# Kernel tuning notes

Measured on AMD Instinct MI355X. Metric: run time of the kernel, lower is better.

The kernel has to match this reference:

```python
import jax, jax.numpy as jnp
import numpy as np

B, T, DM, DK = 8, 2048, 1024, 64

def setup_inputs() -> dict:
    key = jax.random.key(0)
    kx, kk, kq, kv = jax.random.split(key, 4)
    s = 1.0 / np.sqrt(DM)
    return {
        "x": jax.random.normal(kx, (B, T, DM), dtype=jnp.float32),
        "Wk": jax.random.normal(kk, (DM, DK), dtype=jnp.float32) * s,
        "Wq": jax.random.normal(kq, (DM, DK), dtype=jnp.float32) * s,
        "Wv": jax.random.normal(kv, (DM, DK), dtype=jnp.float32) * s,
    }

def reference(x, Wk, Wq, Wv):
    # q, k, v: [B, T, DK]
    k = x @ Wk
    q = x @ Wq
    v = x @ Wv
    # NOTE: original module does NOT scale by 1/sqrt(dk)
    wei = jnp.einsum('btd,bsd->bts', q, k)          # [B, T, T]
    mask = jnp.tril(jnp.ones((x.shape[1], x.shape[1]), dtype=bool))
    wei = jnp.where(mask, wei, -jnp.inf)
    wei = jax.nn.softmax(wei, axis=-1)
    return wei @ v                                   # [B, T, DK]
```

## Files before the change

### kernel.cpp

```cpp
#include <hip/hip_runtime.h>
#include <hip/hip_bf16.h>

typedef unsigned short u16;
typedef __bf16 bf16x8 __attribute__((ext_vector_type(8)));
typedef _Float16 f16x8 __attribute__((ext_vector_type(8)));
typedef float f32x4 __attribute__((ext_vector_type(4)));

#define DEVINL __device__ __forceinline__

static constexpr int Bc = 8, Tc = 2048;

DEVINL u16 f2bf(float f) {
  unsigned u = __builtin_bit_cast(unsigned, f);
  unsigned r = u + 0x7fffu + ((u >> 16) & 1u);
  return (u16)(r >> 16);
}
DEVINL float bf2f(u16 h) {
  unsigned u = ((unsigned)h) << 16;
  return __builtin_bit_cast(float, u);
}

DEVINL bf16x8 lds_ld8(const u16* p, int row, int col) {
  return *(const bf16x8*)&p[row * 64 + (col ^ ((row & 7) << 3))];
}
DEVINL f16x8 lds_ld8h(const u16* p, int row, int col) {
  return *(const f16x8*)&p[row * 64 + (col ^ ((row & 7) << 3))];
}

__global__ __launch_bounds__(256) void build_wt(const float* __restrict__ Wk,
                                                const float* __restrict__ Wq,
                                                const float* __restrict__ Wv,
                                                u16* __restrict__ wt_s) {
  int idx = blockIdx.x * 256 + threadIdx.x;
  int ch = idx / 12288;
  int rem = idx - ch * 12288;
  int c = rem >> 6, kc = rem & 63;
  int k = ch * 64 + (kc ^ ((c & 7) << 3));
  const float* W = (c < 64) ? Wk : (c < 128 ? Wq : Wv);
  _Float16 h = (_Float16)W[k * 64 + (c & 63)];
  wt_s[idx] = __builtin_bit_cast(u16, h);
}

__global__ __launch_bounds__(256, 2) void proj_kernel(const float* __restrict__ x,
                                                      const u16* __restrict__ wt_s,
                                                      u16* __restrict__ kb,
                                                      u16* __restrict__ qb,
                                                      u16* __restrict__ vt) {
  __shared__ u16 wl[2][192 * 64];
  __shared__ u16 xl[2][32 * 64];
  const int t = threadIdx.x;
  const int w = t >> 6, lane = t & 63;
  const int l16 = lane & 15, lhi = lane >> 4;
  const int rb = blockIdx.x * 32;
  const int cb = w * 48;
  const int sr = t >> 3, sc = (t & 7) * 8;
  const f32x4* xrow = (const f32x4*)(x + (size_t)(rb + sr) * 1024 + sc);

  f32x4 acc[2][3];
#pragma unroll
  for (int a = 0; a < 2; ++a)
#pragma unroll
    for (int c = 0; c < 3; ++c) acc[a][c] = (f32x4){0.f, 0.f, 0.f, 0.f};

#define STAGE_WT(S, CH)                                                        \
  {                                                                            \
    const u16* src = wt_s + (size_t)(CH) * 12288 + t * 8;                      \
    u16* dst = &wl[S][t * 8];                                                  \
    _Pragma("unroll") for (int i = 0; i < 6; ++i)                              \
      __builtin_amdgcn_global_load_lds(                                        \
          (const __attribute__((address_space(1))) unsigned int*)(src + i * 2048), \
          (__attribute__((address_space(3))) unsigned int*)(dst + i * 2048),   \
          16, 0, 0);                                                           \
  }

#define CVT_STORE(S, F0, F1)                                                   \
  {                                                                            \
    union { _Float16 h[8]; uint4 v; } p_;                                      \
    _Pragma("unroll") for (int j = 0; j < 4; ++j) {                            \
      p_.h[j] = (_Float16)(F0)[j];                                             \
      p_.h[4 + j] = (_Float16)(F1)[j];                                         \
    }                                                                          \
    *(uint4*)&xl[S][sr * 64 + (sc ^ ((sr & 7) << 3))] = p_.v;                  \
  }

#define COMPUTE(S)                                                             \
  _Pragma("unroll") for (int kk = 0; kk < 2; ++kk) {                           \
    f16x8 a0 = lds_ld8h(xl[S], l16, kk * 32 + lhi * 8);                        \
    f16x8 a1 = lds_ld8h(xl[S], 16 + l16, kk * 32 + lhi * 8);                   \
    _Pragma("unroll") for (int tc = 0; tc < 3; ++tc) {                         \
      int c_ = cb + tc * 16 + l16;                                             \
      f16x8 bf = *(const f16x8*)&wl[S][c_ * 64 + ((kk * 32 + lhi * 8) ^ ((c_ & 7) << 3))]; \
      acc[0][tc] = __builtin_amdgcn_mfma_f32_16x16x32_f16(a0, bf, acc[0][tc], 0, 0, 0); \
      acc[1][tc] = __builtin_amdgcn_mfma_f32_16x16x32_f16(a1, bf, acc[1][tc], 0, 0, 0); \
    }                                                                          \
  }

  STAGE_WT(0, 0);
  {
    f32x4 A0 = __builtin_nontemporal_load(xrow);
    f32x4 A1 = __builtin_nontemporal_load(xrow + 1);
    CVT_STORE(0, A0, A1);
  }
  __syncthreads();

#pragma unroll 2
  for (int ch = 0; ch < 16; ++ch) {
    const int cur = ch & 1, nxt = cur ^ 1;
    f32x4 A0, A1;
    if (ch + 1 < 16) {
      STAGE_WT(nxt, ch + 1);
      A0 = __builtin_nontemporal_load(xrow + (ch + 1) * 16);
      A1 = __builtin_nontemporal_load(xrow + (ch + 1) * 16 + 1);
    }
    COMPUTE(cur);
    if (ch + 1 < 16) {
      CVT_STORE(nxt, A0, A1);
      __syncthreads();
    }
  }
#undef STAGE_WT
#undef CVT_STORE
#undef COMPUTE

#pragma unroll
  for (int ri = 0; ri < 2; ++ri) {
#pragma unroll
    for (int tc = 0; tc < 3; ++tc) {
      int gc = cb + tc * 16 + l16;
      int cc = gc & 63;
      int row = rb + ri * 16 + lhi * 4;
#pragma unroll
      for (int i = 0; i < 4; ++i) {
        float f = acc[ri][tc][i];
        int r = row + i;
        if (gc < 64) {
          _Float16 h = (_Float16)f;
          kb[(size_t)r * 64 + cc] = __builtin_bit_cast(u16, h);
        } else if (gc < 128) {
          _Float16 h = (_Float16)f;
          qb[(size_t)r * 64 + cc] = __builtin_bit_cast(u16, h);
        } else {
          int bb = r >> 11, tp = r & 2047;
          vt[((size_t)bb * 64 + cc) * 2048 + tp] = f2bf(f);
        }
      }
    }
  }
}

__global__ __launch_bounds__(256, 2) void attn_kernel(const u16* __restrict__ qb,
                                                      const u16* __restrict__ kb,
                                                      const u16* __restrict__ vt,
                                                      float* __restrict__ out) {
  __shared__ u16 p_l[4][2][1024];
  __shared__ float om[4][32][64];
  __shared__ float ml[4][2][32];

  const int t = threadIdx.x, w = t >> 6, lane = t & 63;
  const int l16 = lane & 15, lhi = lane >> 4;
  const int b = blockIdx.x & 7, j = 63 - (blockIdx.x >> 3);
  const int ntt = (j + 2) >> 1;
  const size_t qrow = (size_t)b * 2048 + j * 32;

  f16x8 aq[2][2];
#pragma unroll
  for (int rs = 0; rs < 2; ++rs)
#pragma unroll
    for (int kk = 0; kk < 2; ++kk) {
      size_t qo = (qrow + rs * 16 + l16) * 64 + kk * 32 + lhi * 8;
      aq[rs][kk] = *(const f16x8*)(qb + qo);
    }

  f32x4 o[2][4];
  float m_r[2][4], l_r[2][4];
#pragma unroll
  for (int rs = 0; rs < 2; ++rs)
#pragma unroll
    for (int i = 0; i < 4; ++i) {
      o[rs][i] = (f32x4){0.f, 0.f, 0.f, 0.f};
      m_r[rs][i] = -3.0e38f; l_r[rs][i] = 0.f;
    }

  for (int tk = w; tk < ntt; tk += 4) {
    const int kvb = tk * 64;
    const size_t kbase = ((size_t)b * 2048 + kvb) * 64;

    f32x4 sa[2][4];
#pragma unroll
    for (int t4 = 0; t4 < 4; ++t4) {
      size_t kr = kbase + (size_t)(t4 * 16 + l16) * 64 + lhi * 8;
      f16x8 kf0 = *(const f16x8*)(kb + kr);
      f16x8 kf1 = *(const f16x8*)(kb + kr + 32);
#pragma unroll
      for (int rs = 0; rs < 2; ++rs) {
        f32x4 s = (f32x4){0.f, 0.f, 0.f, 0.f};
        s = __builtin_amdgcn_mfma_f32_16x16x32_f16(aq[rs][0], kf0, s, 0, 0, 0);
        s = __builtin_amdgcn_mfma_f32_16x16x32_f16(aq[rs][1], kf1, s, 0, 0, 0);
        sa[rs][t4] = s;
      }
    }

    bf16x8 vv[4][2];
#pragma unroll
    for (int t4 = 0; t4 < 4; ++t4) {
      size_t vr = ((size_t)b * 64 + t4 * 16 + l16) * 2048 + kvb + lhi * 8;
      vv[t4][0] = *(const bf16x8*)(vt + vr);
      vv[t4][1] = *(const bf16x8*)(vt + vr + 32);
    }

    if (tk == ntt - 1) {
#pragma unroll
      for (int rs = 0; rs < 2; ++rs) {
        int qr = j * 32 + rs * 16 + lhi * 4;
#pragma unroll
        for (int t4 = 0; t4 < 4; ++t4) {
          int col = kvb + t4 * 16 + l16;
#pragma unroll
          for (int i = 0; i < 4; ++i)
            if (col > qr + i) sa[rs][t4][i] = -1e30f;
        }
      }
    }

#pragma unroll
    for (int rs = 0; rs < 2; ++rs) {
      float pf[4][4];
#pragma unroll
      for (int i = 0; i < 4; ++i) {
        float tm = fmaxf(fmaxf(sa[rs][0][i], sa[rs][1][i]), fmaxf(sa[rs][2][i], sa[rs][3][i]));
#pragma unroll
        for (int d = 1; d < 16; d <<= 1) tm = fmaxf(tm, __shfl_xor(tm, d));
        float mn = fmaxf(m_r[rs][i], tm);
        float scl = __expf(m_r[rs][i] - mn);
        float rsum = 0.f;
#pragma unroll
        for (int t4 = 0; t4 < 4; ++t4) {
          float p = __expf(sa[rs][t4][i] - mn);
          pf[t4][i] = p;
          rsum += p;
        }
#pragma unroll
        for (int d = 1; d < 16; d <<= 1) rsum += __shfl_xor(rsum, d);
        l_r[rs][i] = l_r[rs][i] * scl + rsum;
        m_r[rs][i] = mn;
#pragma unroll
        for (int t4 = 0; t4 < 4; ++t4) o[rs][t4][i] *= scl;
      }

      u16* pw = (u16*)p_l[w][rs];
#pragma unroll
      for (int i = 0; i < 4; ++i) {
        int rr = lhi * 4 + i;
#pragma unroll
        for (int t4 = 0; t4 < 4; ++t4) {
          int col = t4 * 16 + l16;
          pw[rr * 64 + (col ^ ((rr & 7) << 3))] = f2bf(pf[t4][i]);
        }
      }
#pragma unroll
      for (int kk = 0; kk < 2; ++kk) {
        bf16x8 ap = lds_ld8(pw, l16, kk * 32 + lhi * 8);
#pragma unroll
        for (int t4 = 0; t4 < 4; ++t4)
          o[rs][t4] = __builtin_amdgcn_mfma_f32_16x16x32_bf16(ap, vv[t4][kk], o[rs][t4], 0, 0, 0);
      }
    }
  }

#pragma unroll
  for (int rs = 0; rs < 2; ++rs)
#pragma unroll
    for (int t4 = 0; t4 < 4; ++t4) {
      int col = t4 * 16 + l16;
#pragma unroll
      for (int i = 0; i < 4; ++i)
        om[w][rs * 16 + lhi * 4 + i][col] = o[rs][t4][i];
    }
  if (l16 == 0) {
#pragma unroll
    for (int rs = 0; rs < 2; ++rs)
#pragma unroll
      for (int i = 0; i < 4; ++i) {
        int r = rs * 16 + lhi * 4 + i;
        ml[w][0][r] = m_r[rs][i];
        ml[w][1][r] = l_r[rs][i];
      }
  }
  __syncthreads();

  {
    int r = t >> 3, c0 = (t & 7) * 8;
    float m0 = ml[0][0][r], m1 = ml[1][0][r], m2 = ml[2][0][r], m3 = ml[3][0][r];
    float M = fmaxf(fmaxf(m0, m1), fmaxf(m2, m3));
    float a0 = __expf(m0 - M), a1 = __expf(m1 - M);
    float a2 = __expf(m2 - M), a3 = __expf(m3 - M);
    float den = ml[0][1][r] * a0 + ml[1][1][r] * a1 + ml[2][1][r] * a2 + ml[3][1][r] * a3;
    float inv = 1.f / den;
    float* og = out + (qrow + r) * 64 + c0;
#pragma unroll
    for (int cc = 0; cc < 8; ++cc) {
      float v = om[0][r][c0 + cc] * a0 + om[1][r][c0 + cc] * a1 +
                om[2][r][c0 + cc] * a2 + om[3][r][c0 + cc] * a3;
      og[cc] = v * inv;
    }
  }
}

extern "C" void kernel_launch(void* const* d_in, const int* in_sizes, int n_in,
                              void* d_out, int out_size, void* d_ws, size_t ws_size,
                              hipStream_t stream) {
  const float* x  = (const float*)d_in[0];
  const float* Wk = (const float*)d_in[1];
  const float* Wq = (const float*)d_in[2];
  const float* Wv = (const float*)d_in[3];
  float* out = (float*)d_out;

  const size_t QKV = (size_t)Bc * Tc * 64;
  char* w = (char*)d_ws;
  u16* kb   = (u16*)w;               w += QKV * 2;
  u16* qb   = (u16*)w;               w += QKV * 2;
  u16* vt   = (u16*)w;               w += QKV * 2;
  u16* wt_s = (u16*)w;               w += (size_t)16 * 192 * 64 * 2;

  build_wt<<<768, 256, 0, stream>>>(Wk, Wq, Wv, wt_s);
  proj_kernel<<<512, 256, 0, stream>>>(x, wt_s, kb, qb, vt);
  attn_kernel<<<512, 256, 0, stream>>>(qb, kb, vt, out);
}
```

Measured before the change: 67.34 us.

## Compute transposed scores so P stays in registers for the PV MFMA

Swaps the MFMA operand order so each lane holds scores for a single query row across four key positions. The probabilities can then feed a 16x16x16 f16 MFMA directly as register fragments, which removes the per-tile LDS round trip for P. V is now stored as f16 instead of bf16 to match. The row max and sum now need only two cross-lane shuffles instead of four, and the output staging buffer is padded to reduce bank conflicts. The cost is twice as many smaller MFMAs and narrower 4-element V loads.

```diff
diff --git a/kernel.cpp b/kernel.cpp
--- a/kernel.cpp
+++ b/kernel.cpp
@@ -4,6 +4,7 @@
 typedef unsigned short u16;
 typedef __bf16 bf16x8 __attribute__((ext_vector_type(8)));
 typedef _Float16 f16x8 __attribute__((ext_vector_type(8)));
+typedef _Float16 f16x4 __attribute__((ext_vector_type(4)));
 typedef float f32x4 __attribute__((ext_vector_type(4)));
 
 #define DEVINL __device__ __forceinline__
@@ -15,14 +16,7 @@
   unsigned r = u + 0x7fffu + ((u >> 16) & 1u);
   return (u16)(r >> 16);
 }
-DEVINL float bf2f(u16 h) {
-  unsigned u = ((unsigned)h) << 16;
-  return __builtin_bit_cast(float, u);
-}
-
-DEVINL bf16x8 lds_ld8(const u16* p, int row, int col) {
-  return *(const bf16x8*)&p[row * 64 + (col ^ ((row & 7) << 3))];
-}
+
 DEVINL f16x8 lds_ld8h(const u16* p, int row, int col) {
   return *(const f16x8*)&p[row * 64 + (col ^ ((row & 7) << 3))];
 }
@@ -133,15 +127,15 @@
       for (int i = 0; i < 4; ++i) {
         float f = acc[ri][tc][i];
         int r = row + i;
+        _Float16 h = (_Float16)f;
+        u16 hb = __builtin_bit_cast(u16, h);
         if (gc < 64) {
-          _Float16 h = (_Float16)f;
-          kb[(size_t)r * 64 + cc] = __builtin_bit_cast(u16, h);
+          kb[(size_t)r * 64 + cc] = hb;
         } else if (gc < 128) {
-          _Float16 h = (_Float16)f;
-          qb[(size_t)r * 64 + cc] = __builtin_bit_cast(u16, h);
+          qb[(size_t)r * 64 + cc] = hb;
         } else {
           int bb = r >> 11, tp = r & 2047;
-          vt[((size_t)bb * 64 + cc) * 2048 + tp] = f2bf(f);
+          vt[((size_t)bb * 64 + cc) * 2048 + tp] = hb;
         }
       }
     }
@@ -152,8 +146,7 @@
                                                       const u16* __restrict__ kb,
                                                       const u16* __restrict__ vt,
                                                       float* __restrict__ out) {
-  __shared__ u16 p_l[4][2][1024];
-  __shared__ float om[4][32][64];
+  __shared__ float om[4][32][65];
   __shared__ float ml[4][2][32];
 
   const int t = threadIdx.x, w = t >> 6, lane = t & 63;
@@ -172,14 +165,13 @@
     }
 
   f32x4 o[2][4];
-  float m_r[2][4], l_r[2][4];
-#pragma unroll
-  for (int rs = 0; rs < 2; ++rs)
-#pragma unroll
-    for (int i = 0; i < 4; ++i) {
-      o[rs][i] = (f32x4){0.f, 0.f, 0.f, 0.f};
-      m_r[rs][i] = -3.0e38f; l_r[rs][i] = 0.f;
-    }
+  float m_r[2], l_r[2];
+#pragma unroll
+  for (int rs = 0; rs < 2; ++rs) {
+    m_r[rs] = -3.0e38f; l_r[rs] = 0.f;
+#pragma unroll
+    for (int d4 = 0; d4 < 4; ++d4) o[rs][d4] = (f32x4){0.f, 0.f, 0.f, 0.f};
+  }
 
   for (int tk = w; tk < ntt; tk += 4) {
     const int kvb = tk * 64;
@@ -194,97 +186,87 @@
 #pragma unroll
       for (int rs = 0; rs < 2; ++rs) {
         f32x4 s = (f32x4){0.f, 0.f, 0.f, 0.f};
-        s = __builtin_amdgcn_mfma_f32_16x16x32_f16(aq[rs][0], kf0, s, 0, 0, 0);
-        s = __builtin_amdgcn_mfma_f32_16x16x32_f16(aq[rs][1], kf1, s, 0, 0, 0);
+        s = __builtin_amdgcn_mfma_f32_16x16x32_f16(kf0, aq[rs][0], s, 0, 0, 0);
+        s = __builtin_amdgcn_mfma_f32_16x16x32_f16(kf1, aq[rs][1], s, 0, 0, 0);
         sa[rs][t4] = s;
       }
     }
 
-    bf16x8 vv[4][2];
-#pragma unroll
-    for (int t4 = 0; t4 < 4; ++t4) {
-      size_t vr = ((size_t)b * 64 + t4 * 16 + l16) * 2048 + kvb + lhi * 8;
-      vv[t4][0] = *(const bf16x8*)(vt + vr);
-      vv[t4][1] = *(const bf16x8*)(vt + vr + 32);
+    f16x4 va[4][4];
+#pragma unroll
+    for (int d4 = 0; d4 < 4; ++d4) {
+      size_t vr = ((size_t)b * 64 + d4 * 16 + l16) * 2048 + kvb + lhi * 4;
+#pragma unroll
+      for (int t4 = 0; t4 < 4; ++t4)
+        va[d4][t4] = *(const f16x4*)(vt + vr + t4 * 16);
     }
 
     if (tk == ntt - 1) {
 #pragma unroll
       for (int rs = 0; rs < 2; ++rs) {
-        int qr = j * 32 + rs * 16 + lhi * 4;
+        int q = j * 32 + rs * 16 + l16;
 #pragma unroll
         for (int t4 = 0; t4 < 4; ++t4) {
-          int col = kvb + t4 * 16 + l16;
+          int kvr = kvb + t4 * 16 + lhi * 4;
 #pragma unroll
           for (int i = 0; i < 4; ++i)
-            if (col > qr + i) sa[rs][t4][i] = -1e30f;
+            if (kvr + i > q) sa[rs][t4][i] = -1e30f;
         }
       }
     }
 
+    f16x4 pfrag[2][4];
 #pragma unroll
     for (int rs = 0; rs < 2; ++rs) {
-      float pf[4][4];
-#pragma unroll
-      for (int i = 0; i < 4; ++i) {
-        float tm = fmaxf(fmaxf(sa[rs][0][i], sa[rs][1][i]), fmaxf(sa[rs][2][i], sa[rs][3][i]));
-#pragma unroll
-        for (int d = 1; d < 16; d <<= 1) tm = fmaxf(tm, __shfl_xor(tm, d));
-        float mn = fmaxf(m_r[rs][i], tm);
-        float scl = __expf(m_r[rs][i] - mn);
-        float rsum = 0.f;
-#pragma unroll
-        for (int t4 = 0; t4 < 4; ++t4) {
-          float p = __expf(sa[rs][t4][i] - mn);
-          pf[t4][i] = p;
-          rsum += p;
-        }
-#pragma unroll
-        for (int d = 1; d < 16; d <<= 1) rsum += __shfl_xor(rsum, d);
-        l_r[rs][i] = l_r[rs][i] * scl + rsum;
-        m_r[rs][i] = mn;
-#pragma unroll
-        for (int t4 = 0; t4 < 4; ++t4) o[rs][t4][i] *= scl;
+      float tm = fmaxf(fmaxf(fmaxf(sa[rs][0][0], sa[rs][0][1]), fmaxf(sa[rs][0][2], sa[rs][0][3])),
+                       fmaxf(fmaxf(sa[rs][1][0], sa[rs][1][1]), fmaxf(sa[rs][1][2], sa[rs][1][3])));
+      float tm2 = fmaxf(fmaxf(fmaxf(sa[rs][2][0], sa[rs][2][1]), fmaxf(sa[rs][2][2], sa[rs][2][3])),
+                        fmaxf(fmaxf(sa[rs][3][0], sa[rs][3][1]), fmaxf(sa[rs][3][2], sa[rs][3][3])));
+      tm = fmaxf(tm, tm2);
+      tm = fmaxf(tm, __shfl_xor(tm, 16));
+      tm = fmaxf(tm, __shfl_xor(tm, 32));
+      float mn = fmaxf(m_r[rs], tm);
+      float scl = __expf(m_r[rs] - mn);
+      float rsum = 0.f;
+#pragma unroll
+      for (int t4 = 0; t4 < 4; ++t4) {
+        float p0 = __expf(sa[rs][t4][0] - mn);
+        float p1 = __expf(sa[rs][t4][1] - mn);
+        float p2 = __expf(sa[rs][t4][2] - mn);
+        float p3 = __expf(sa[rs][t4][3] - mn);
+        rsum += (p0 + p1) + (p2 + p3);
+        pfrag[rs][t4] = (f16x4){(_Float16)p0, (_Float16)p1, (_Float16)p2, (_Float16)p3};
       }
-
-      u16* pw = (u16*)p_l[w][rs];
-#pragma unroll
-      for (int i = 0; i < 4; ++i) {
-        int rr = lhi * 4 + i;
-#pragma unroll
-        for (int t4 = 0; t4 < 4; ++t4) {
-          int col = t4 * 16 + l16;
-          pw[rr * 64 + (col ^ ((rr & 7) << 3))] = f2bf(pf[t4][i]);
-        }
-      }
-#pragma unroll
-      for (int kk = 0; kk < 2; ++kk) {
-        bf16x8 ap = lds_ld8(pw, l16, kk * 32 + lhi * 8);
-#pragma unroll
-        for (int t4 = 0; t4 < 4; ++t4)
-          o[rs][t4] = __builtin_amdgcn_mfma_f32_16x16x32_bf16(ap, vv[t4][kk], o[rs][t4], 0, 0, 0);
-      }
-    }
+      rsum += __shfl_xor(rsum, 16);
+      rsum += __shfl_xor(rsum, 32);
+      l_r[rs] = l_r[rs] * scl + rsum;
+      m_r[rs] = mn;
+#pragma unroll
+      for (int d4 = 0; d4 < 4; ++d4) o[rs][d4] *= scl;
+    }
+
+#pragma unroll
+    for (int rs = 0; rs < 2; ++rs)
+#pragma unroll
+      for (int t4 = 0; t4 < 4; ++t4)
+#pragma unroll
+        for (int d4 = 0; d4 < 4; ++d4)
+          o[rs][d4] = __builtin_amdgcn_mfma_f32_16x16x16f16(va[d4][t4], pfrag[rs][t4], o[rs][d4], 0, 0, 0);
   }
 
 #pragma unroll
   for (int rs = 0; rs < 2; ++rs)
 #pragma unroll
-    for (int t4 = 0; t4 < 4; ++t4) {
-      int col = t4 * 16 + l16;
+    for (int d4 = 0; d4 < 4; ++d4)
 #pragma unroll
       for (int i = 0; i < 4; ++i)
-        om[w][rs * 16 + lhi * 4 + i][col] = o[rs][t4][i];
-    }
-  if (l16 == 0) {
-#pragma unroll
-    for (int rs = 0; rs < 2; ++rs)
-#pragma unroll
-      for (int i = 0; i < 4; ++i) {
-        int r = rs * 16 + lhi * 4 + i;
-        ml[w][0][r] = m_r[rs][i];
-        ml[w][1][r] = l_r[rs][i];
-      }
+        om[w][rs * 16 + l16][d4 * 16 + lhi * 4 + i] = o[rs][d4][i];
+  if (lane < 16) {
+#pragma unroll
+    for (int rs = 0; rs < 2; ++rs) {
+      ml[w][0][rs * 16 + lane] = m_r[rs];
+      ml[w][1][rs * 16 + lane] = l_r[rs];
+    }
   }
   __syncthreads();
 
```

After: 74.07 us. 10.0% more time.
